# Optimization experiments

Hardware: AMD Instinct MI355X
Metric: run time of the kernel (lower is better)

The kernel has to match this reference:

```python
import jax, jax.numpy as jnp
import numpy as np

NUM_HEADS = 4
GROUPS = 8
EPS = 1e-5


def setup_inputs() -> dict:
    key = jax.random.key(0)
    ks = jax.random.split(key, 8)
    B, C, H, W = 8, 512, 64, 64
    L, E = 77, 768
    std = 0.02
    return {
        "x": jax.random.normal(ks[0], (B, C, H, W), jnp.float32),
        "text_emb": jax.random.normal(ks[1], (B, L, E), jnp.float32),
        "attention_mask": jax.random.randint(ks[2], (B, L), 0, 2, jnp.int32),
        "Wq_w": jax.random.normal(ks[3], (C, C), jnp.float32) * std,
        "Wq_b": jnp.zeros((C,), jnp.float32),
        "Wk_w": jax.random.normal(ks[4], (C, E), jnp.float32) * std,
        "Wk_b": jnp.zeros((C,), jnp.float32),
        "Wv_w": jax.random.normal(ks[5], (C, E), jnp.float32) * std,
        "Wv_b": jnp.zeros((C,), jnp.float32),
        "gn_scale": jnp.ones((C,), jnp.float32),
        "gn_bias": jnp.zeros((C,), jnp.float32),
    }


def reference(x, text_emb, attention_mask, Wq_w, Wq_b, Wk_w, Wk_b, Wv_w, Wv_b, gn_scale, gn_bias):
    B, C, H, W = x.shape
    dh = C // NUM_HEADS
    scale = dh ** -0.5

    # [B, HW, C] queries from image features
    x_flat = x.reshape(B, C, H * W).transpose(0, 2, 1)
    Q = x_flat @ Wq_w.T + Wq_b                 # [B, S, C]
    K = text_emb @ Wk_w.T + Wk_b               # [B, L, C]
    V = text_emb @ Wv_w.T + Wv_b               # [B, L, C]

    def split_heads(t):
        Bt, T, _ = t.shape
        return t.reshape(Bt, T, NUM_HEADS, dh).transpose(0, 2, 1, 3)  # [B, h, T, dh]

    Qh, Kh, Vh = split_heads(Q), split_heads(K), split_heads(V)

    scores = jnp.einsum("bhqd,bhkd->bhqk", Qh, Kh) * scale  # [B, h, S, L]
    mask = (attention_mask == 0)[:, None, None, :]
    scores = jnp.where(mask, -jnp.inf, scores)
    probs = jax.nn.softmax(scores, axis=-1)
    # dropout layers are identity in eval mode
    attn = jnp.einsum("bhqk,bhkd->bhqd", probs, Vh)          # [B, h, S, dh]

    out = attn.transpose(0, 2, 1, 3).reshape(B, H * W, C)    # [B, S, C]
    out = out.transpose(0, 2, 1).reshape(B, C, H, W)

    # GroupNorm(8 groups, affine) over (C/G, H, W) per group
    g = out.reshape(B, GROUPS, -1)
    mean = g.mean(axis=-1, keepdims=True)
    var = g.var(axis=-1, keepdims=True)
    g = (g - mean) * jax.lax.rsqrt(var + EPS)
    out = g.reshape(B, C, H, W) * gn_scale[None, :, None, None] + gn_bias[None, :, None, None]
    return out
```

## Files before the change

kernel.cpp:

```cpp
#include <hip/hip_runtime.h>
#include <hip/hip_bf16.h>
#include <cstdint>


typedef __attribute__((ext_vector_type(8))) short short8;
typedef __attribute__((ext_vector_type(4))) short short4v;
typedef __attribute__((ext_vector_type(4))) float f32x4;

#define DEV __device__ __forceinline__

DEV float bf2f(unsigned short u){ union{uint32_t i; float f;} x; x.i = ((uint32_t)u) << 16; return x.f; }
DEV unsigned short f2bf(float f){ __hip_bfloat16 h = __float2bfloat16(f); return *reinterpret_cast<unsigned short*>(&h); }
DEV short8 ld8(const unsigned short* p){ return *reinterpret_cast<const short8*>(p); }
DEV f32x4 ldf4(const float* p){ return *reinterpret_cast<const f32x4*>(p); }

#if defined(__has_builtin)
#if __has_builtin(__builtin_amdgcn_global_load_lds)
#define HAVE_ASYNC_LDS 1
#endif
#endif

__global__ __launch_bounds__(256) void k_fat(const float* __restrict__ x,
                                             unsigned short* __restrict__ xTt,
                                             const float* __restrict__ text,
                                             const float* __restrict__ Wk,
                                             const float* __restrict__ Wkb,
                                             const float* __restrict__ Wv,
                                             const float* __restrict__ Wvb,
                                             unsigned short* __restrict__ wsK,
                                             unsigned short* __restrict__ wsVt,
                                             const float* __restrict__ Wq,
                                             unsigned short* __restrict__ wsWqT,
                                             int b0, int s_base, int slen, int SB){
  __shared__ unsigned short U[16896];
  const int tid = threadIdx.x;
  const int bx = blockIdx.x, by = blockIdx.y, bz = blockIdx.z;
  const int bg = b0 + bz;

  if (bx >= 3){
    const int cc = by, c0 = cc * 64;
    const int tile = bx - 3;
    const int s0 = s_base + tile * 256;
    {
      const int r = tid >> 2, sub = tid & 3;
      const float* src = &x[((size_t)(bg * 512 + c0 + r)) * 4096 + s0 + sub * 64];
      f32x4 rv[16];
      #pragma unroll
      for (int i = 0; i < 16; ++i) rv[i] = ldf4(src + i * 4);
      unsigned short* drow = &U[r * 264 + sub * 64];
      #pragma unroll
      for (int i = 0; i < 8; ++i){
        short8 v;
        #pragma unroll
        for (int j = 0; j < 4; ++j){ v[j] = (short)f2bf(rv[2*i][j]); v[j + 4] = (short)f2bf(rv[2*i+1][j]); }
        *reinterpret_cast<short8*>(drow + i * 8) = v;
      }
    }
    __syncthreads();
    {
      const int j = tid;
      unsigned short v[64];
      #pragma unroll
      for (int r = 0; r < 64; ++r) v[r] = U[r * 264 + j];
      const int sloc = tile * 256 + j;
      unsigned short* dst = &xTt[(((size_t)bz * 8 + cc) * slen + sloc) * 64];
      #pragma unroll
      for (int g = 0; g < 8; ++g)
        *reinterpret_cast<short8*>(dst + g * 8) = *reinterpret_cast<short8*>(&v[g * 8]);
    }
  } else if (bx < 2){
    unsigned short* At = U;
    unsigned short* Bt = U + 5760;
    const int wave = tid >> 6, lane = tid & 63;
    const int m16 = lane & 15, quad = lane >> 4;
    const int uc = bx * 8 + by;
    const int u0 = uc * 64;
    const bool isK = (u0 < 512);
    const float* W  = isK ? Wk  : Wv;
    const float* Wb = isK ? Wkb : Wvb;
    const int c0 = u0 & 511;
    const int c  = c0 + wave * 16 + m16;

    int srow[9], se4[9]; bool sA[9], sval[9];
    #pragma unroll
    for (int it = 0; it < 9; ++it){
      int slot = tid + it * 256;
      if (slot < 1280){ sA[it] = true;  srow[it] = slot >> 4;          se4[it] = (slot & 15) * 4; sval[it] = (srow[it] < 77); }
      else            { sA[it] = false; srow[it] = (slot - 1280) >> 4; se4[it] = ((slot - 1280) & 15) * 4; sval[it] = true; }
    }
    f32x4 preg[9];
    auto issue = [&](int kc){
      const int e0 = kc * 64;
      #pragma unroll
      for (int it = 0; it < 9; ++it){
        if (sA[it])
          preg[it] = sval[it] ? ldf4(&text[((size_t)(bg * 77 + srow[it])) * 768 + e0 + se4[it]])
                              : (f32x4){0.f, 0.f, 0.f, 0.f};
        else
          preg[it] = ldf4(&W[((size_t)(c0 + srow[it])) * 768 + e0 + se4[it]]);
      }
    };
    auto write_lds = [&](){
      #pragma unroll
      for (int it = 0; it < 9; ++it){
        short4v o;
        #pragma unroll
        for (int j = 0; j < 4; ++j) o[j] = (short)f2bf(preg[it][j]);
        if (sA[it]) *reinterpret_cast<short4v*>(&At[srow[it] * 72 + se4[it]]) = o;
        else        *reinterpret_cast<short4v*>(&Bt[srow[it] * 72 + se4[it]]) = o;
      }
    };

    f32x4 acc[5];
    #pragma unroll
    for (int mt = 0; mt < 5; ++mt) acc[mt] = (f32x4){0.f, 0.f, 0.f, 0.f};
    issue(0);
    for (int kc = 0; kc < 12; ++kc){
      write_lds();
      __syncthreads();
      if (kc < 11) issue(kc + 1);
      #pragma unroll
      for (int kk = 0; kk < 64; kk += 32){
        short8 bf_ = *reinterpret_cast<const short8*>(&Bt[(wave * 16 + m16) * 72 + kk + quad * 8]);
        #pragma unroll
        for (int mt = 0; mt < 5; ++mt){
          short8 af_ = *reinterpret_cast<const short8*>(&At[(mt * 16 + m16) * 72 + kk + quad * 8]);
          acc[mt] = __builtin_amdgcn_mfma_f32_16x16x32_bf16(af_, bf_, acc[mt], 0, 0, 0);
        }
      }
      __syncthreads();
    }
    const float bias = Wb[c];
    if (isK){
      #pragma unroll
      for (int mt = 0; mt < 5; ++mt)
        #pragma unroll
        for (int r = 0; r < 4; ++r){
          int l = mt * 16 + quad * 4 + r;
          if (l < 77) wsK[((size_t)(bz * 77 + l)) * 512 + c] = f2bf(acc[mt][r] + bias);
        }
    } else {
      unsigned short* vr = &wsVt[((size_t)(bz * 512 + c)) * 96];
      #pragma unroll
      for (int mt = 0; mt < 5; ++mt){
        short4v pk;
        #pragma unroll
        for (int r = 0; r < 4; ++r) pk[r] = (short)f2bf(acc[mt][r] + bias);
        *reinterpret_cast<short4v*>(&vr[mt * 16 + quad * 4]) = pk;
      }
      short4v z = {};
      *reinterpret_cast<short4v*>(&vr[80 + quad * 4]) = z;
    }
  } else {
    unsigned short* t = U;
    const int nb = 8 * SB;
    const int p  = by + bz * 8;
    for (int tile = p; tile < 64; tile += nb){
      const int ti = tile >> 3, tj = tile & 7;
      {
        const int r = tid >> 2, sub = tid & 3;
        const float* src = &Wq[((size_t)(tj * 64 + r)) * 512 + ti * 64 + sub * 16];
        f32x4 rv[4];
        #pragma unroll
        for (int i = 0; i < 4; ++i) rv[i] = ldf4(src + i * 4);
        unsigned short* drow = &t[r * 72 + sub * 16];
        #pragma unroll
        for (int i = 0; i < 2; ++i){
          short8 v;
          #pragma unroll
          for (int j = 0; j < 4; ++j){ v[j] = (short)f2bf(rv[2*i][j]); v[j + 4] = (short)f2bf(rv[2*i+1][j]); }
          *reinterpret_cast<short8*>(drow + i * 8) = v;
        }
      }
      __syncthreads();
      #pragma unroll
      for (int it = 0; it < 2; ++it){
        int slot = tid + it * 256;
        int j = slot >> 3, i8 = slot & 7;
        short8 v;
        #pragma unroll
        for (int q = 0; q < 8; ++q)
          v[q] = (short)t[(i8 * 8 + q) * 72 + (j & 63)];
        *reinterpret_cast<short8*>(&wsWqT[((size_t)(ti * 64 + j)) * 512 + tj * 64 + i8 * 8]) = v;
      }
      __syncthreads();
    }
  }
}

__global__ __launch_bounds__(256) void k1b(const unsigned short* __restrict__ wsWqT,
                                           const unsigned short* __restrict__ wsK,
                                           const float* __restrict__ Wqb,
                                           unsigned short* __restrict__ wsKWq,
                                           float* __restrict__ kbias){
  const int tid = threadIdx.x;
  const int wave = tid >> 6, lane = tid & 63;
  const int m16 = lane & 15, quad = lane >> 4;
  const int cq = blockIdx.x, h = blockIdx.y, bz = blockIdx.z;
  const int cbase = cq * 128 + wave * 32;

  f32x4 acc[2][5];
  #pragma unroll
  for (int mt = 0; mt < 2; ++mt)
    #pragma unroll
    for (int nt = 0; nt < 5; ++nt) acc[mt][nt] = (f32x4){0.f, 0.f, 0.f, 0.f};

  #pragma unroll
  for (int ks = 0; ks < 4; ++ks){
    short8 aw[2];
    #pragma unroll
    for (int mt = 0; mt < 2; ++mt)
      aw[mt] = ld8(&wsWqT[(size_t)(cbase + mt * 16 + m16) * 512 + h * 128 + ks * 32 + quad * 8]);
    #pragma unroll
    for (int nt = 0; nt < 5; ++nt){
      int l = nt * 16 + m16;
      short8 bk = {};
      if (l < 77) bk = ld8(&wsK[((size_t)(bz * 77 + l)) * 512 + h * 128 + ks * 32 + quad * 8]);
      #pragma unroll
      for (int mt = 0; mt < 2; ++mt)
        acc[mt][nt] = __builtin_amdgcn_mfma_f32_16x16x32_bf16(aw[mt], bk, acc[mt][nt], 0, 0, 0);
    }
  }
  #pragma unroll
  for (int mt = 0; mt < 2; ++mt)
    #pragma unroll
    for (int nt = 0; nt < 5; ++nt){
      int l = nt * 16 + m16;
      short4v pk;
      #pragma unroll
      for (int r = 0; r < 4; ++r) pk[r] = (short)f2bf(acc[mt][nt][r]);
      *reinterpret_cast<short4v*>(&wsKWq[((size_t)((bz * 4 + h) * 80 + l)) * 512 + cbase + mt * 16 + quad * 4]) = pk;
    }
  if (cq == 0 && tid < 80){
    int l = tid;
    float kb = 0.f;
    if (l < 77){
      #pragma unroll
      for (int d = 0; d < 128; d += 8){
        short8 kv = ld8(&wsK[((size_t)(bz * 77 + l)) * 512 + h * 128 + d]);
        f32x4 wa = ldf4(&Wqb[h * 128 + d]);
        f32x4 wb = ldf4(&Wqb[h * 128 + d + 4]);
        #pragma unroll
        for (int j = 0; j < 4; ++j){
          kb += bf2f((unsigned short)kv[j]) * wa[j];
          kb += bf2f((unsigned short)kv[j + 4]) * wb[j];
        }
      }
    }
    kbias[(bz * 4 + h) * 80 + l] = kb;
  }
}

__global__ __launch_bounds__(256, 4) void k2_attn(const unsigned short* __restrict__ xTt,
                                                  const unsigned short* __restrict__ wsKWq,
                                                  const unsigned short* __restrict__ wsVt,
                                                  const int* __restrict__ amask,
                                                  const float* __restrict__ kbias,
                                                  float* __restrict__ out,
                                                  unsigned short* __restrict__ outTmp,
                                                  float* __restrict__ gnacc,
                                                  int b0, int s_base, int slen, int useTmp){
  __shared__ unsigned short arena[13312];
  __shared__ float maskf[96];
  unsigned short* Pt = arena;

  const int tid = threadIdx.x;
  const int wave = tid >> 6, lane = tid & 63;
  const int m16 = lane & 15, quad = lane >> 4;
  const int bz = blockIdx.x, h = blockIdx.y, st = blockIdx.z;
  const int bg = b0 + bz;
  const int s_glob = s_base + st * 128;
  const int R0 = (wave >> 1) * 64, C0 = (wave & 1) * 64;
  const int sw0 = wave * 32;
  const float scale = 0.08838834764831845f;

  if (tid < 96){
    int l = tid;
    float mbv = -30000.f;
    if (l < 77 && amask[bg * 77 + l] != 0) mbv = kbias[(bz * 4 + h) * 80 + l] * scale;
    maskf[l] = mbv;
  }

  const unsigned short* Abase = wsKWq + (size_t)((bz * 4 + h) * 80) * 512;
  const unsigned short* Bb    = xTt + (size_t)(bz * 8) * slen * 64;
  const int srow0 = st * 128 + sw0;

  f32x4 acc2[5][2];
  #pragma unroll
  for (int mt = 0; mt < 5; ++mt){ acc2[mt][0] = (f32x4){0.f,0.f,0.f,0.f}; acc2[mt][1] = (f32x4){0.f,0.f,0.f,0.f}; }

  auto stageA = [&](int kc, int buf){
    const int sbase = buf * 5120;
    #pragma unroll
    for (int it = 0; it < 3; ++it){
      const int ubase = it * 256 + wave * 64;
      if (ubase < 640){
        const int u = ubase + lane;
        int l = u >> 3, pos = (u & 7) ^ (l & 7);
        const unsigned short* src = Abase + (size_t)l * 512 + kc * 64 + pos * 8;
#ifdef HAVE_ASYNC_LDS
        __builtin_amdgcn_global_load_lds((const __attribute__((address_space(1))) void*)src,
                                         (__attribute__((address_space(3))) void*)&arena[sbase + ubase * 8],
                                         16, 0, 0);
#else
        *reinterpret_cast<short8*>(&arena[sbase + u * 8]) = ld8(src);
#endif
      }
    }
  };

  short8 Breg[2][4];
  auto loadB = [&](int kc, int buf){
    const unsigned short* Bc = Bb + ((size_t)kc * slen + srow0) * 64;
    #pragma unroll
    for (int nt = 0; nt < 2; ++nt)
      #pragma unroll
      for (int kk = 0; kk < 2; ++kk)
        Breg[buf][nt * 2 + kk] = ld8(&Bc[(size_t)(nt * 16 + m16) * 64 + kk * 32 + quad * 8]);
  };

  auto compute = [&](int buf){
    const int ab = buf * 5120;
    #pragma unroll
    for (int kk = 0; kk < 2; ++kk){
      short8 af[5];
      #pragma unroll
      for (int mt = 0; mt < 5; ++mt){
        int l = mt * 16 + m16;
        int p = (kk * 4 + quad) ^ (l & 7);
        af[mt] = *reinterpret_cast<const short8*>(&arena[ab + l * 64 + p * 8]);
      }
      #pragma unroll
      for (int mt = 0; mt < 5; ++mt)
        #pragma unroll
        for (int nt = 0; nt < 2; ++nt)
          acc2[mt][nt] = __builtin_amdgcn_mfma_f32_16x16x32_bf16(af[mt], Breg[buf][nt * 2 + kk], acc2[mt][nt], 0, 0, 0);
    }
  };

  stageA(0, 0);
  loadB(0, 0);
  __syncthreads();
  #pragma unroll
  for (int kc = 0; kc < 8; ++kc){
    if (kc < 7){ stageA(kc + 1, (kc + 1) & 1); loadB(kc + 1, (kc + 1) & 1); }
    compute(kc & 1);
    __syncthreads();
  }

  const unsigned short* Vb = wsVt + (size_t)(bz * 512 + h * 128) * 96;
  short8 av0[4];
  #pragma unroll
  for (int mt = 0; mt < 4; ++mt)
    av0[mt] = ld8(&Vb[(size_t)(R0 + mt * 16 + m16) * 96 + quad * 8]);

  {
    float mb[5][4];
    #pragma unroll
    for (int mt = 0; mt < 5; ++mt)
      #pragma unroll
      for (int r = 0; r < 4; ++r) mb[mt][r] = maskf[mt * 16 + quad * 4 + r];
    #pragma unroll
    for (int nt = 0; nt < 2; ++nt){
      float sv[5][4]; float mx = -3e38f;
      #pragma unroll
      for (int mt = 0; mt < 5; ++mt)
        #pragma unroll
        for (int r = 0; r < 4; ++r){
          float v = acc2[mt][nt][r] * scale + mb[mt][r];
          sv[mt][r] = v; mx = fmaxf(mx, v);
        }
      mx = fmaxf(mx, __shfl_xor(mx, 16)); mx = fmaxf(mx, __shfl_xor(mx, 32));
      float sum = 0.f;
      #pragma unroll
      for (int mt = 0; mt < 5; ++mt)
        #pragma unroll
        for (int r = 0; r < 4; ++r){ float e = __expf(sv[mt][r] - mx); sv[mt][r] = e; sum += e; }
      sum += __shfl_xor(sum, 16); sum += __shfl_xor(sum, 32);
      float inv = 1.0f / sum;
      int sl = sw0 + nt * 16 + m16;
      #pragma unroll
      for (int mt = 0; mt < 5; ++mt){
        short4v pk;
        #pragma unroll
        for (int r = 0; r < 4; ++r) pk[r] = (short)f2bf(sv[mt][r] * inv);
        *reinterpret_cast<short4v*>(&Pt[sl * 104 + mt * 16 + quad * 4]) = pk;
      }
      short4v z = {};
      *reinterpret_cast<short4v*>(&Pt[sl * 104 + 80 + quad * 4]) = z;
    }
  }
  __syncthreads();

  f32x4 acc3[4][4];
  #pragma unroll
  for (int mt = 0; mt < 4; ++mt)
    #pragma unroll
    for (int nt = 0; nt < 4; ++nt) acc3[mt][nt] = (f32x4){0.f, 0.f, 0.f, 0.f};
  #pragma unroll
  for (int ks = 0; ks < 3; ++ks){
    short8 av[4], bp[4];
    #pragma unroll
    for (int mt = 0; mt < 4; ++mt)
      av[mt] = (ks == 0) ? av0[mt]
                         : ld8(&Vb[(size_t)(R0 + mt * 16 + m16) * 96 + ks * 32 + quad * 8]);
    #pragma unroll
    for (int nt = 0; nt < 4; ++nt)
      bp[nt] = *reinterpret_cast<const short8*>(&Pt[(C0 + nt * 16 + m16) * 104 + ks * 32 + quad * 8]);
    #pragma unroll
    for (int mt = 0; mt < 4; ++mt)
      #pragma unroll
      for (int nt = 0; nt < 4; ++nt)
        acc3[mt][nt] = __builtin_amdgcn_mfma_f32_16x16x32_bf16(av[mt], bp[nt], acc3[mt][nt], 0, 0, 0);
  }

  float sum = 0.f, ssq = 0.f;
  #pragma unroll
  for (int mt = 0; mt < 4; ++mt)
    #pragma unroll
    for (int nt = 0; nt < 4; ++nt)
      #pragma unroll
      for (int r = 0; r < 4; ++r){
        float v = acc3[mt][nt][r];
        sum += v; ssq += v * v;
      }
  #pragma unroll
  for (int off = 1; off < 64; off <<= 1){ sum += __shfl_xor(sum, off); ssq += __shfl_xor(ssq, off); }
  if (lane == 0){
    int g = h * 2 + (R0 >> 6);
    atomicAdd(&gnacc[(bg * 8 + g) * 2],     sum);
    atomicAdd(&gnacc[(bg * 8 + g) * 2 + 1], ssq);
  }

  if (useTmp){
    __syncthreads();
    float* T = reinterpret_cast<float*>(arena);
    const int TS = 132;
    #pragma unroll
    for (int p = 0; p < 4; ++p){
      if ((R0 >> 6) == (p >> 1)){
        #pragma unroll
        for (int mt2 = 0; mt2 < 2; ++mt2){
          int mt = (p & 1) * 2 + mt2;
          #pragma unroll
          for (int nt = 0; nt < 4; ++nt)
            #pragma unroll
            for (int r = 0; r < 4; ++r)
              T[(mt2 * 16 + quad * 4 + r) * TS + C0 + nt * 16 + m16] = acc3[mt][nt][r];
        }
      }
      __syncthreads();
      #pragma unroll
      for (int it = 0; it < 4; ++it){
        int row = wave * 8 + it * 2 + (lane >> 5);
        int c = h * 128 + p * 32 + row;
        int sc = (lane & 31) * 4;
        f32x4 v = *reinterpret_cast<const f32x4*>(&T[row * TS + sc]);
        short4v o;
        #pragma unroll
        for (int j = 0; j < 4; ++j) o[j] = (short)f2bf(v[j]);
        *reinterpret_cast<short4v*>(&outTmp[(size_t)(bg * 512 + c) * 4096 + s_glob + sc]) = o;
      }
      __syncthreads();
    }
  } else {
    #pragma unroll
    for (int mt = 0; mt < 4; ++mt)
      #pragma unroll
      for (int nt = 0; nt < 4; ++nt){
        int sidx = s_glob + C0 + nt * 16 + m16;
        #pragma unroll
        for (int r = 0; r < 4; ++r){
          int d = h * 128 + R0 + mt * 16 + quad * 4 + r;
          out[(size_t)(bg * 512 + d) * 4096 + sidx] = acc3[mt][nt][r];
        }
      }
  }
}

__global__ __launch_bounds__(256) void k3_gn_b(const unsigned short* __restrict__ tmp,
                                               float* __restrict__ out,
                                               const float* __restrict__ gnacc,
                                               const float* __restrict__ gns,
                                               const float* __restrict__ gnb){
  const int bx = blockIdx.x;
  const int b = bx >> 9, c = bx & 511;
  const int g = c >> 6;
  const float s  = gnacc[(b * 8 + g) * 2];
  const float ss = gnacc[(b * 8 + g) * 2 + 1];
  const float invN = 1.f / 262144.f;
  const float mean = s * invN;
  const float var  = ss * invN - mean * mean;
  const float rstd = rsqrtf(fmaxf(var, 0.f) + 1e-5f);
  const float a  = rstd * gns[c];
  const float bb = gnb[c] - mean * a;
  const size_t base = (size_t)bx * 4096;
  const unsigned short* src = &tmp[base + threadIdx.x * 16];
  float* dst = &out[base + threadIdx.x * 16];
  short8 v0 = ld8(src), v1 = ld8(src + 8);
  #pragma unroll
  for (int k = 0; k < 2; ++k){
    short8 v = k ? v1 : v0;
    f32x4 o0, o1;
    #pragma unroll
    for (int j = 0; j < 4; ++j){
      o0[j] = bf2f((unsigned short)v[j])     * a + bb;
      o1[j] = bf2f((unsigned short)v[j + 4]) * a + bb;
    }
    *reinterpret_cast<f32x4*>(dst + k * 8)     = o0;
    *reinterpret_cast<f32x4*>(dst + k * 8 + 4) = o1;
  }
}

__global__ __launch_bounds__(256) void k3_gn(float* __restrict__ out,
                                             const float* __restrict__ gnacc,
                                             const float* __restrict__ gns,
                                             const float* __restrict__ gnb){
  const int bx = blockIdx.x;
  const int b = bx >> 9, c = bx & 511;
  const int g = c >> 6;
  const float s  = gnacc[(b * 8 + g) * 2];
  const float ss = gnacc[(b * 8 + g) * 2 + 1];
  const float invN = 1.f / 262144.f;
  const float mean = s * invN;
  const float var  = ss * invN - mean * mean;
  const float rstd = rsqrtf(fmaxf(var, 0.f) + 1e-5f);
  const float a  = rstd * gns[c];
  const float bb = gnb[c] - mean * a;
  const size_t base = (size_t)bx * 4096;
  #pragma unroll
  for (int p = 0; p < 4; ++p){
    size_t off = base + p * 1024 + threadIdx.x * 4;
    f32x4 v = ldf4(&out[off]);
    f32x4 o;
    #pragma unroll
    for (int j = 0; j < 4; ++j) o[j] = v[j] * a + bb;
    *reinterpret_cast<f32x4*>(&out[off]) = o;
  }
}

extern "C" void kernel_launch(void* const* d_in, const int* in_sizes, int n_in,
                              void* d_out, int out_size, void* d_ws, size_t ws_size,
                              hipStream_t stream){
  (void)in_sizes; (void)n_in; (void)out_size;
  const float* x    = (const float*)d_in[0];
  const float* text = (const float*)d_in[1];
  const int*   am   = (const int*)d_in[2];
  const float* Wq   = (const float*)d_in[3];
  const float* Wqb  = (const float*)d_in[4];
  const float* Wk   = (const float*)d_in[5];
  const float* Wkb  = (const float*)d_in[6];
  const float* Wv   = (const float*)d_in[7];
  const float* Wvb  = (const float*)d_in[8];
  const float* gns  = (const float*)d_in[9];
  const float* gnb  = (const float*)d_in[10];
  float* out = (float*)d_out;

  auto need = [](int SB, int SLEN) -> size_t {
    return 512ull + 524288ull + (size_t)SB * 506112ull + (size_t)SB * SLEN * 1024ull;
  };
  int SB = 8, SLEN = 4096;
  if      (ws_size >= need(8, 4096)) { SB = 8; SLEN = 4096; }
  else if (ws_size >= need(4, 4096)) { SB = 4; SLEN = 4096; }
  else if (ws_size >= need(2, 4096)) { SB = 2; SLEN = 4096; }
  else if (ws_size >= need(1, 4096)) { SB = 1; SLEN = 4096; }
  else if (ws_size >= need(1, 1024)) { SB = 1; SLEN = 1024; }
  else                               { SB = 1; SLEN = 256;  }

  const size_t tmpBytes = 8ull * 512 * 4096 * 2;
  const int useTmp = (SB == 8 && SLEN == 4096 && ws_size >= need(8, 4096) + tmpBytes) ? 1 : 0;

  uint8_t* ws = (uint8_t*)d_ws;
  float*          gnacc = (float*)ws;
  unsigned short* wsWqT = (unsigned short*)(ws + 512);
  unsigned short* wsK   = wsWqT + 512 * 512;
  unsigned short* wsVt  = wsK  + (size_t)SB * 77 * 512;
  unsigned short* wsKWq = wsVt + (size_t)SB * 512 * 96;
  float*          kbias = (float*)(wsKWq + (size_t)SB * 4 * 80 * 512);
  unsigned short* xTt   = (unsigned short*)(kbias + (size_t)SB * 4 * 80);
  unsigned short* outTmp = xTt + (size_t)SB * 8 * SLEN * 64;

  hipMemsetAsync(gnacc, 0, 128 * sizeof(float), stream);
  for (int b0 = 0; b0 < 8; b0 += SB){
    for (int s_base = 0; s_base < 4096; s_base += SLEN){
      const int NT = SLEN >> 8;
      k_fat<<<dim3(NT + 3, 8, SB), 256, 0, stream>>>(x, xTt, text, Wk, Wkb, Wv, Wvb,
                                                     wsK, wsVt, Wq, wsWqT, b0, s_base, SLEN, SB);
      if (s_base == 0)
        k1b<<<dim3(4, 4, SB), 256, 0, stream>>>(wsWqT, wsK, Wqb, wsKWq, kbias);
      k2_attn<<<dim3(SB, 4, SLEN / 128), 256, 0, stream>>>(xTt, wsKWq, wsVt, am, kbias,
                                                           out, outTmp, gnacc,
                                                           b0, s_base, SLEN, useTmp);
    }
  }
  if (useTmp)
    k3_gn_b<<<4096, 256, 0, stream>>>(outTmp, out, gnacc, gns, gnb);
  else
    k3_gn<<<4096, 256, 0, stream>>>(out, gnacc, gns, gnb);
}
```

Baseline: 121.1 us.

## Process two heads per attention block to reuse loaded query tiles

Each k2_attn block now handles two heads instead of one. The xTt query tile is loaded into registers once and fed to the score MFMAs of both heads, which halves how often B is read from global memory. The grid's head dimension halves, LDS per block grows to hold two A stages, and launch bounds drop to 2 blocks per CU because the doubled accumulators raise register pressure. The price is lower occupancy and a serial per-head softmax/PV/epilogue section inside each block.

```diff
diff --git a/kernel.cpp b/kernel.cpp
--- a/kernel.cpp
+++ b/kernel.cpp
@@ -251,7 +251,7 @@
   }
 }
 
-__global__ __launch_bounds__(256, 4) void k2_attn(const unsigned short* __restrict__ xTt,
+__global__ __launch_bounds__(256, 2) void k2_attn(const unsigned short* __restrict__ xTt,
                                                   const unsigned short* __restrict__ wsKWq,
                                                   const unsigned short* __restrict__ wsVt,
                                                   const int* __restrict__ amask,
@@ -260,52 +260,61 @@
                                                   unsigned short* __restrict__ outTmp,
                                                   float* __restrict__ gnacc,
                                                   int b0, int s_base, int slen, int useTmp){
-  __shared__ unsigned short arena[13312];
-  __shared__ float maskf[96];
+  __shared__ unsigned short arena[20480];
+  __shared__ float maskf[2][96];
   unsigned short* Pt = arena;
 
   const int tid = threadIdx.x;
   const int wave = tid >> 6, lane = tid & 63;
   const int m16 = lane & 15, quad = lane >> 4;
-  const int bz = blockIdx.x, h = blockIdx.y, st = blockIdx.z;
+  const int bz = blockIdx.x, hp = blockIdx.y, st = blockIdx.z;
   const int bg = b0 + bz;
   const int s_glob = s_base + st * 128;
   const int R0 = (wave >> 1) * 64, C0 = (wave & 1) * 64;
   const int sw0 = wave * 32;
   const float scale = 0.08838834764831845f;
 
-  if (tid < 96){
-    int l = tid;
+  if ((tid & 127) < 96){
+    int hh = tid >> 7, l = tid & 127;
+    int h = hp * 2 + hh;
     float mbv = -30000.f;
     if (l < 77 && amask[bg * 77 + l] != 0) mbv = kbias[(bz * 4 + h) * 80 + l] * scale;
-    maskf[l] = mbv;
-  }
-
-  const unsigned short* Abase = wsKWq + (size_t)((bz * 4 + h) * 80) * 512;
-  const unsigned short* Bb    = xTt + (size_t)(bz * 8) * slen * 64;
+    maskf[hh][l] = mbv;
+  }
+
+  const unsigned short* Ab[2];
+  #pragma unroll
+  for (int hh = 0; hh < 2; ++hh)
+    Ab[hh] = wsKWq + (size_t)((bz * 4 + hp * 2 + hh) * 80) * 512;
+  const unsigned short* Bb = xTt + (size_t)(bz * 8) * slen * 64;
   const int srow0 = st * 128 + sw0;
 
-  f32x4 acc2[5][2];
-  #pragma unroll
-  for (int mt = 0; mt < 5; ++mt){ acc2[mt][0] = (f32x4){0.f,0.f,0.f,0.f}; acc2[mt][1] = (f32x4){0.f,0.f,0.f,0.f}; }
+  f32x4 acc2[2][5][2];
+  #pragma unroll
+  for (int hh = 0; hh < 2; ++hh)
+    #pragma unroll
+    for (int mt = 0; mt < 5; ++mt){
+      acc2[hh][mt][0] = (f32x4){0.f,0.f,0.f,0.f};
+      acc2[hh][mt][1] = (f32x4){0.f,0.f,0.f,0.f};
+    }
 
   auto stageA = [&](int kc, int buf){
-    const int sbase = buf * 5120;
-    #pragma unroll
-    for (int it = 0; it < 3; ++it){
+    const int sbase = buf * 10240;
+    #pragma unroll
+    for (int it = 0; it < 5; ++it){
       const int ubase = it * 256 + wave * 64;
-      if (ubase < 640){
-        const int u = ubase + lane;
-        int l = u >> 3, pos = (u & 7) ^ (l & 7);
-        const unsigned short* src = Abase + (size_t)l * 512 + kc * 64 + pos * 8;
+      const int u = ubase + lane;
+      const int hh = (u >= 640) ? 1 : 0;
+      const int uu = u - hh * 640;
+      int l = uu >> 3, pos = (uu & 7) ^ (l & 7);
+      const unsigned short* src = Ab[hh] + (size_t)l * 512 + kc * 64 + pos * 8;
 #ifdef HAVE_ASYNC_LDS
-        __builtin_amdgcn_global_load_lds((const __attribute__((address_space(1))) void*)src,
-                                         (__attribute__((address_space(3))) void*)&arena[sbase + ubase * 8],
-                                         16, 0, 0);
+      __builtin_amdgcn_global_load_lds((const __attribute__((address_space(1))) void*)src,
+                                       (__attribute__((address_space(3))) void*)&arena[sbase + ubase * 8],
+                                       16, 0, 0);
 #else
-        *reinterpret_cast<short8*>(&arena[sbase + u * 8]) = ld8(src);
+      *reinterpret_cast<short8*>(&arena[sbase + u * 8]) = ld8(src);
 #endif
-      }
     }
   };
 
@@ -320,21 +329,24 @@
   };
 
   auto compute = [&](int buf){
-    const int ab = buf * 5120;
+    const int ab = buf * 10240;
     #pragma unroll
     for (int kk = 0; kk < 2; ++kk){
-      short8 af[5];
-      #pragma unroll
-      for (int mt = 0; mt < 5; ++mt){
-        int l = mt * 16 + m16;
-        int p = (kk * 4 + quad) ^ (l & 7);
-        af[mt] = *reinterpret_cast<const short8*>(&arena[ab + l * 64 + p * 8]);
-      }
-      #pragma unroll
-      for (int mt = 0; mt < 5; ++mt)
-        #pragma unroll
-        for (int nt = 0; nt < 2; ++nt)
-          acc2[mt][nt] = __builtin_amdgcn_mfma_f32_16x16x32_bf16(af[mt], Breg[buf][nt * 2 + kk], acc2[mt][nt], 0, 0, 0);
+      #pragma unroll
+      for (int hh = 0; hh < 2; ++hh){
+        short8 af[5];
+        #pragma unroll
+        for (int mt = 0; mt < 5; ++mt){
+          int l = mt * 16 + m16;
+          int p = (kk * 4 + quad) ^ (l & 7);
+          af[mt] = *reinterpret_cast<const short8*>(&arena[ab + hh * 5120 + l * 64 + p * 8]);
+        }
+        #pragma unroll
+        for (int mt = 0; mt < 5; ++mt)
+          #pragma unroll
+          for (int nt = 0; nt < 2; ++nt)
+            acc2[hh][mt][nt] = __builtin_amdgcn_mfma_f32_16x16x32_bf16(af[mt], Breg[buf][nt * 2 + kk], acc2[hh][mt][nt], 0, 0, 0);
+      }
     }
   };
 
@@ -348,133 +360,138 @@
     __syncthreads();
   }
 
-  const unsigned short* Vb = wsVt + (size_t)(bz * 512 + h * 128) * 96;
-  short8 av0[4];
-  #pragma unroll
-  for (int mt = 0; mt < 4; ++mt)
-    av0[mt] = ld8(&Vb[(size_t)(R0 + mt * 16 + m16) * 96 + quad * 8]);
-
-  {
-    float mb[5][4];
-    #pragma unroll
-    for (int mt = 0; mt < 5; ++mt)
-      #pragma unroll
-      for (int r = 0; r < 4; ++r) mb[mt][r] = maskf[mt * 16 + quad * 4 + r];
-    #pragma unroll
-    for (int nt = 0; nt < 2; ++nt){
-      float sv[5][4]; float mx = -3e38f;
+  #pragma unroll
+  for (int hh = 0; hh < 2; ++hh){
+    const int h = hp * 2 + hh;
+    const unsigned short* Vb = wsVt + (size_t)(bz * 512 + h * 128) * 96;
+    short8 av0[4];
+    #pragma unroll
+    for (int mt = 0; mt < 4; ++mt)
+      av0[mt] = ld8(&Vb[(size_t)(R0 + mt * 16 + m16) * 96 + quad * 8]);
+
+    {
+      float mb[5][4];
       #pragma unroll
       for (int mt = 0; mt < 5; ++mt)
         #pragma unroll
+        for (int r = 0; r < 4; ++r) mb[mt][r] = maskf[hh][mt * 16 + quad * 4 + r];
+      #pragma unroll
+      for (int nt = 0; nt < 2; ++nt){
+        float sv[5][4]; float mx = -3e38f;
+        #pragma unroll
+        for (int mt = 0; mt < 5; ++mt)
+          #pragma unroll
+          for (int r = 0; r < 4; ++r){
+            float v = acc2[hh][mt][nt][r] * scale + mb[mt][r];
+            sv[mt][r] = v; mx = fmaxf(mx, v);
+          }
+        mx = fmaxf(mx, __shfl_xor(mx, 16)); mx = fmaxf(mx, __shfl_xor(mx, 32));
+        float sum = 0.f;
+        #pragma unroll
+        for (int mt = 0; mt < 5; ++mt)
+          #pragma unroll
+          for (int r = 0; r < 4; ++r){ float e = __expf(sv[mt][r] - mx); sv[mt][r] = e; sum += e; }
+        sum += __shfl_xor(sum, 16); sum += __shfl_xor(sum, 32);
+        float inv = 1.0f / sum;
+        int sl = sw0 + nt * 16 + m16;
+        #pragma unroll
+        for (int mt = 0; mt < 5; ++mt){
+          short4v pk;
+          #pragma unroll
+          for (int r = 0; r < 4; ++r) pk[r] = (short)f2bf(sv[mt][r] * inv);
+          *reinterpret_cast<short4v*>(&Pt[sl * 104 + mt * 16 + quad * 4]) = pk;
+        }
+        short4v z = {};
+        *reinterpret_cast<short4v*>(&Pt[sl * 104 + 80 + quad * 4]) = z;
+      }
+    }
+    __syncthreads();
+
+    f32x4 acc3[4][4];
+    #pragma unroll
+    for (int mt = 0; mt < 4; ++mt)
+      #pragma unroll
+      for (int nt = 0; nt < 4; ++nt) acc3[mt][nt] = (f32x4){0.f, 0.f, 0.f, 0.f};
+    #pragma unroll
+    for (int ks = 0; ks < 3; ++ks){
+      short8 av[4], bp[4];
+      #pragma unroll
+      for (int mt = 0; mt < 4; ++mt)
+        av[mt] = (ks == 0) ? av0[mt]
+                           : ld8(&Vb[(size_t)(R0 + mt * 16 + m16) * 96 + ks * 32 + quad * 8]);
+      #pragma unroll
+      for (int nt = 0; nt < 4; ++nt)
+        bp[nt] = *reinterpret_cast<const short8*>(&Pt[(C0 + nt * 16 + m16) * 104 + ks * 32 + quad * 8]);
+      #pragma unroll
+      for (int mt = 0; mt < 4; ++mt)
+        #pragma unroll
+        for (int nt = 0; nt < 4; ++nt)
+          acc3[mt][nt] = __builtin_amdgcn_mfma_f32_16x16x32_bf16(av[mt], bp[nt], acc3[mt][nt], 0, 0, 0);
+    }
+
+    float sum = 0.f, ssq = 0.f;
+    #pragma unroll
+    for (int mt = 0; mt < 4; ++mt)
+      #pragma unroll
+      for (int nt = 0; nt < 4; ++nt)
+        #pragma unroll
         for (int r = 0; r < 4; ++r){
-          float v = acc2[mt][nt][r] * scale + mb[mt][r];
-          sv[mt][r] = v; mx = fmaxf(mx, v);
-        }
-      mx = fmaxf(mx, __shfl_xor(mx, 16)); mx = fmaxf(mx, __shfl_xor(mx, 32));
-      float sum = 0.f;
-      #pragma unroll
-      for (int mt = 0; mt < 5; ++mt)
-        #pragma unroll
-        for (int r = 0; r < 4; ++r){ float e = __expf(sv[mt][r] - mx); sv[mt][r] = e; sum += e; }
-      sum += __shfl_xor(sum, 16); sum += __shfl_xor(sum, 32);
-      float inv = 1.0f / sum;
-      int sl = sw0 + nt * 16 + m16;
-      #pragma unroll
-      for (int mt = 0; mt < 5; ++mt){
-        short4v pk;
-        #pragma unroll
-        for (int r = 0; r < 4; ++r) pk[r] = (short)f2bf(sv[mt][r] * inv);
-        *reinterpret_cast<short4v*>(&Pt[sl * 104 + mt * 16 + quad * 4]) = pk;
-      }
-      short4v z = {};
-      *reinterpret_cast<short4v*>(&Pt[sl * 104 + 80 + quad * 4]) = z;
-    }
-  }
-  __syncthreads();
-
-  f32x4 acc3[4][4];
-  #pragma unroll
-  for (int mt = 0; mt < 4; ++mt)
-    #pragma unroll
-    for (int nt = 0; nt < 4; ++nt) acc3[mt][nt] = (f32x4){0.f, 0.f, 0.f, 0.f};
-  #pragma unroll
-  for (int ks = 0; ks < 3; ++ks){
-    short8 av[4], bp[4];
-    #pragma unroll
-    for (int mt = 0; mt < 4; ++mt)
-      av[mt] = (ks == 0) ? av0[mt]
-                         : ld8(&Vb[(size_t)(R0 + mt * 16 + m16) * 96 + ks * 32 + quad * 8]);
-    #pragma unroll
-    for (int nt = 0; nt < 4; ++nt)
-      bp[nt] = *reinterpret_cast<const short8*>(&Pt[(C0 + nt * 16 + m16) * 104 + ks * 32 + quad * 8]);
-    #pragma unroll
-    for (int mt = 0; mt < 4; ++mt)
-      #pragma unroll
-      for (int nt = 0; nt < 4; ++nt)
-        acc3[mt][nt] = __builtin_amdgcn_mfma_f32_16x16x32_bf16(av[mt], bp[nt], acc3[mt][nt], 0, 0, 0);
-  }
-
-  float sum = 0.f, ssq = 0.f;
-  #pragma unroll
-  for (int mt = 0; mt < 4; ++mt)
-    #pragma unroll
-    for (int nt = 0; nt < 4; ++nt)
-      #pragma unroll
-      for (int r = 0; r < 4; ++r){
-        float v = acc3[mt][nt][r];
-        sum += v; ssq += v * v;
-      }
-  #pragma unroll
-  for (int off = 1; off < 64; off <<= 1){ sum += __shfl_xor(sum, off); ssq += __shfl_xor(ssq, off); }
-  if (lane == 0){
-    int g = h * 2 + (R0 >> 6);
-    atomicAdd(&gnacc[(bg * 8 + g) * 2],     sum);
-    atomicAdd(&gnacc[(bg * 8 + g) * 2 + 1], ssq);
-  }
-
-  if (useTmp){
-    __syncthreads();
-    float* T = reinterpret_cast<float*>(arena);
-    const int TS = 132;
-    #pragma unroll
-    for (int p = 0; p < 4; ++p){
-      if ((R0 >> 6) == (p >> 1)){
-        #pragma unroll
-        for (int mt2 = 0; mt2 < 2; ++mt2){
-          int mt = (p & 1) * 2 + mt2;
-          #pragma unroll
-          for (int nt = 0; nt < 4; ++nt)
+          float v = acc3[mt][nt][r];
+          sum += v; ssq += v * v;
+        }
+    #pragma unroll
+    for (int off = 1; off < 64; off <<= 1){ sum += __shfl_xor(sum, off); ssq += __shfl_xor(ssq, off); }
+    if (lane == 0){
+      int g = h * 2 + (R0 >> 6);
+      atomicAdd(&gnacc[(bg * 8 + g) * 2],     sum);
+      atomicAdd(&gnacc[(bg * 8 + g) * 2 + 1], ssq);
+    }
+
+    if (useTmp){
+      __syncthreads();
+      float* T = reinterpret_cast<float*>(arena);
+      const int TS = 132;
+      #pragma unroll
+      for (int p = 0; p < 4; ++p){
+        if ((R0 >> 6) == (p >> 1)){
+          #pragma unroll
+          for (int mt2 = 0; mt2 < 2; ++mt2){
+            int mt = (p & 1) * 2 + mt2;
             #pragma unroll
-            for (int r = 0; r < 4; ++r)
-              T[(mt2 * 16 + quad * 4 + r) * TS + C0 + nt * 16 + m16] = acc3[mt][nt][r];
-        }
-      }
+            for (int nt = 0; nt < 4; ++nt)
+              #pragma unroll
+              for (int r = 0; r < 4; ++r)
+                T[(mt2 * 16 + quad * 4 + r) * TS + C0 + nt * 16 + m16] = acc3[mt][nt][r];
+          }
+        }
+        __syncthreads();
+        #pragma unroll
+        for (int it = 0; it < 4; ++it){
+          int row = wave * 8 + it * 2 + (lane >> 5);
+          int c = h * 128 + p * 32 + row;
+          int sc = (lane & 31) * 4;
+          f32x4 v = *reinterpret_cast<const f32x4*>(&T[row * TS + sc]);
+          short4v o;
+          #pragma unroll
+          for (int j = 0; j < 4; ++j) o[j] = (short)f2bf(v[j]);
+          *reinterpret_cast<short4v*>(&outTmp[(size_t)(bg * 512 + c) * 4096 + s_glob + sc]) = o;
+        }
+        __syncthreads();
+      }
+    } else {
+      #pragma unroll
+      for (int mt = 0; mt < 4; ++mt)
+        #pragma unroll
+        for (int nt = 0; nt < 4; ++nt){
+          int sidx = s_glob + C0 + nt * 16 + m16;
+          #pragma unroll
+          for (int r = 0; r < 4; ++r){
+            int d = h * 128 + R0 + mt * 16 + quad * 4 + r;
+            out[(size_t)(bg * 512 + d) * 4096 + sidx] = acc3[mt][nt][r];
+          }
+        }
       __syncthreads();
-      #pragma unroll
-      for (int it = 0; it < 4; ++it){
-        int row = wave * 8 + it * 2 + (lane >> 5);
-        int c = h * 128 + p * 32 + row;
-        int sc = (lane & 31) * 4;
-        f32x4 v = *reinterpret_cast<const f32x4*>(&T[row * TS + sc]);
-        short4v o;
-        #pragma unroll
-        for (int j = 0; j < 4; ++j) o[j] = (short)f2bf(v[j]);
-        *reinterpret_cast<short4v*>(&outTmp[(size_t)(bg * 512 + c) * 4096 + s_glob + sc]) = o;
-      }
-      __syncthreads();
-    }
-  } else {
-    #pragma unroll
-    for (int mt = 0; mt < 4; ++mt)
-      #pragma unroll
-      for (int nt = 0; nt < 4; ++nt){
-        int sidx = s_glob + C0 + nt * 16 + m16;
-        #pragma unroll
-        for (int r = 0; r < 4; ++r){
-          int d = h * 128 + R0 + mt * 16 + quad * 4 + r;
-          out[(size_t)(bg * 512 + d) * 4096 + sidx] = acc3[mt][nt][r];
-        }
-      }
+    }
   }
 }
 
@@ -588,7 +605,7 @@
                                                      wsK, wsVt, Wq, wsWqT, b0, s_base, SLEN, SB);
       if (s_base == 0)
         k1b<<<dim3(4, 4, SB), 256, 0, stream>>>(wsWqT, wsK, Wqb, wsKWq, kbias);
-      k2_attn<<<dim3(SB, 4, SLEN / 128), 256, 0, stream>>>(xTt, wsKWq, wsVt, am, kbias,
+      k2_attn<<<dim3(SB, 2, SLEN / 128), 256, 0, stream>>>(xTt, wsKWq, wsVt, am, kbias,
                                                            out, outTmp, gnacc,
                                                            b0, s_base, SLEN, useTmp);
     }
```

New measurement: 117.8 us (median of 2 runs). 2.6% less time.

## Stage full K·Wq tile in LDS once and drop per-chunk barriers in score GEMM

Applied to the files above, without the earlier changes.

The attention kernel now loads the whole 80x512 bf16 K·Wq slab for the head into LDS with one async batch, where before it double-buffered 64-wide chunks with a barrier after each. The B operand (image features) is prefetched four chunks ahead in registers, and the mask bias is computed directly into registers instead of going through shared memory. This removes seven block barriers and the per-chunk staging latency in the QK phase. In exchange, LDS per block grows to about 80KB and the launch bound drops to 2 blocks per CU, which lowers occupancy and raises register pressure.

```diff
diff --git a/kernel.cpp b/kernel.cpp
--- a/kernel.cpp
+++ b/kernel.cpp
@@ -251,7 +251,7 @@
   }
 }
 
-__global__ __launch_bounds__(256, 4) void k2_attn(const unsigned short* __restrict__ xTt,
+__global__ __launch_bounds__(256, 2) void k2_attn(const unsigned short* __restrict__ xTt,
                                                   const unsigned short* __restrict__ wsKWq,
                                                   const unsigned short* __restrict__ wsVt,
                                                   const int* __restrict__ amask,
@@ -260,8 +260,7 @@
                                                   unsigned short* __restrict__ outTmp,
                                                   float* __restrict__ gnacc,
                                                   int b0, int s_base, int slen, int useTmp){
-  __shared__ unsigned short arena[13312];
-  __shared__ float maskf[96];
+  __shared__ unsigned short arena[40960];
   unsigned short* Pt = arena;
 
   const int tid = threadIdx.x;
@@ -274,79 +273,78 @@
   const int sw0 = wave * 32;
   const float scale = 0.08838834764831845f;
 
-  if (tid < 96){
-    int l = tid;
-    float mbv = -30000.f;
-    if (l < 77 && amask[bg * 77 + l] != 0) mbv = kbias[(bz * 4 + h) * 80 + l] * scale;
-    maskf[l] = mbv;
-  }
-
   const unsigned short* Abase = wsKWq + (size_t)((bz * 4 + h) * 80) * 512;
   const unsigned short* Bb    = xTt + (size_t)(bz * 8) * slen * 64;
   const int srow0 = st * 128 + sw0;
 
+  #pragma unroll
+  for (int i = 0; i < 20; ++i){
+    const int ubase = i * 256 + wave * 64;
+    const int u = ubase + lane;
+    const int l = u >> 6, pos = u & 63;
+    const unsigned short* src = Abase + (size_t)l * 512 + (pos ^ (l & 7)) * 8;
+#ifdef HAVE_ASYNC_LDS
+    __builtin_amdgcn_global_load_lds((const __attribute__((address_space(1))) void*)src,
+                                     (__attribute__((address_space(3))) void*)&arena[ubase * 8],
+                                     16, 0, 0);
+#else
+    *reinterpret_cast<short8*>(&arena[u * 8]) = ld8(src);
+#endif
+  }
+
+  short8 Breg[4][4];
+  auto loadB = [&](int kc, int slot){
+    const unsigned short* Bc = Bb + ((size_t)kc * slen + srow0) * 64;
+    #pragma unroll
+    for (int nt = 0; nt < 2; ++nt)
+      #pragma unroll
+      for (int kk = 0; kk < 2; ++kk)
+        Breg[slot][nt * 2 + kk] = ld8(&Bc[(size_t)(nt * 16 + m16) * 64 + kk * 32 + quad * 8]);
+  };
+  #pragma unroll
+  for (int c4 = 0; c4 < 4; ++c4) loadB(c4, c4);
+
+  float mb[5][4];
+  #pragma unroll
+  for (int mt = 0; mt < 5; ++mt)
+    #pragma unroll
+    for (int r = 0; r < 4; ++r){
+      int l = mt * 16 + quad * 4 + r;
+      float v = -30000.f;
+      if (l < 77 && amask[bg * 77 + l] != 0) v = kbias[(bz * 4 + h) * 80 + l] * scale;
+      mb[mt][r] = v;
+    }
+
   f32x4 acc2[5][2];
   #pragma unroll
   for (int mt = 0; mt < 5; ++mt){ acc2[mt][0] = (f32x4){0.f,0.f,0.f,0.f}; acc2[mt][1] = (f32x4){0.f,0.f,0.f,0.f}; }
 
-  auto stageA = [&](int kc, int buf){
-    const int sbase = buf * 5120;
-    #pragma unroll
-    for (int it = 0; it < 3; ++it){
-      const int ubase = it * 256 + wave * 64;
-      if (ubase < 640){
-        const int u = ubase + lane;
-        int l = u >> 3, pos = (u & 7) ^ (l & 7);
-        const unsigned short* src = Abase + (size_t)l * 512 + kc * 64 + pos * 8;
-#ifdef HAVE_ASYNC_LDS
-        __builtin_amdgcn_global_load_lds((const __attribute__((address_space(1))) void*)src,
-                                         (__attribute__((address_space(3))) void*)&arena[sbase + ubase * 8],
-                                         16, 0, 0);
-#else
-        *reinterpret_cast<short8*>(&arena[sbase + u * 8]) = ld8(src);
-#endif
-      }
-    }
-  };
-
-  short8 Breg[2][4];
-  auto loadB = [&](int kc, int buf){
-    const unsigned short* Bc = Bb + ((size_t)kc * slen + srow0) * 64;
-    #pragma unroll
-    for (int nt = 0; nt < 2; ++nt)
-      #pragma unroll
-      for (int kk = 0; kk < 2; ++kk)
-        Breg[buf][nt * 2 + kk] = ld8(&Bc[(size_t)(nt * 16 + m16) * 64 + kk * 32 + quad * 8]);
-  };
-
-  auto compute = [&](int buf){
-    const int ab = buf * 5120;
+  auto compute = [&](int kc, int slot){
     #pragma unroll
     for (int kk = 0; kk < 2; ++kk){
       short8 af[5];
       #pragma unroll
       for (int mt = 0; mt < 5; ++mt){
         int l = mt * 16 + m16;
-        int p = (kk * 4 + quad) ^ (l & 7);
-        af[mt] = *reinterpret_cast<const short8*>(&arena[ab + l * 64 + p * 8]);
+        int gs = (kc * 8 + kk * 4 + quad) ^ (l & 7);
+        af[mt] = *reinterpret_cast<const short8*>(&arena[l * 512 + gs * 8]);
       }
       #pragma unroll
       for (int mt = 0; mt < 5; ++mt)
         #pragma unroll
         for (int nt = 0; nt < 2; ++nt)
-          acc2[mt][nt] = __builtin_amdgcn_mfma_f32_16x16x32_bf16(af[mt], Breg[buf][nt * 2 + kk], acc2[mt][nt], 0, 0, 0);
+          acc2[mt][nt] = __builtin_amdgcn_mfma_f32_16x16x32_bf16(af[mt], Breg[slot][nt * 2 + kk], acc2[mt][nt], 0, 0, 0);
     }
   };
 
-  stageA(0, 0);
-  loadB(0, 0);
   __syncthreads();
-  #pragma unroll
-  for (int kc = 0; kc < 8; ++kc){
-    if (kc < 7){ stageA(kc + 1, (kc + 1) & 1); loadB(kc + 1, (kc + 1) & 1); }
-    compute(kc & 1);
-    __syncthreads();
-  }
+
+  #pragma unroll
+  for (int kc = 0; kc < 4; ++kc) compute(kc, kc);
+  #pragma unroll
+  for (int kc = 4; kc < 8; ++kc) loadB(kc, kc - 4);
+  #pragma unroll
+  for (int kc = 4; kc < 8; ++kc) compute(kc, kc - 4);
 
   const unsigned short* Vb = wsVt + (size_t)(bz * 512 + h * 128) * 96;
   short8 av0[4];
@@ -354,41 +352,36 @@
   for (int mt = 0; mt < 4; ++mt)
     av0[mt] = ld8(&Vb[(size_t)(R0 + mt * 16 + m16) * 96 + quad * 8]);
 
-  {
-    float mb[5][4];
+  __syncthreads();
+
+  #pragma unroll
+  for (int nt = 0; nt < 2; ++nt){
+    float sv[5][4]; float mx = -3e38f;
     #pragma unroll
     for (int mt = 0; mt < 5; ++mt)
       #pragma unroll
-      for (int r = 0; r < 4; ++r) mb[mt][r] = maskf[mt * 16 + quad * 4 + r];
-    #pragma unroll
-    for (int nt = 0; nt < 2; ++nt){
-      float sv[5][4]; float mx = -3e38f;
-      #pragma unroll
-      for (int mt = 0; mt < 5; ++mt)
-        #pragma unroll
-        for (int r = 0; r < 4; ++r){
-          float v = acc2[mt][nt][r] * scale + mb[mt][r];
-          sv[mt][r] = v; mx = fmaxf(mx, v);
-        }
-      mx = fmaxf(mx, __shfl_xor(mx, 16)); mx = fmaxf(mx, __shfl_xor(mx, 32));
-      float sum = 0.f;
-      #pragma unroll
-      for (int mt = 0; mt < 5; ++mt)
-        #pragma unroll
-        for (int r = 0; r < 4; ++r){ float e = __expf(sv[mt][r] - mx); sv[mt][r] = e; sum += e; }
-      sum += __shfl_xor(sum, 16); sum += __shfl_xor(sum, 32);
-      float inv = 1.0f / sum;
-      int sl = sw0 + nt * 16 + m16;
-      #pragma unroll
-      for (int mt = 0; mt < 5; ++mt){
-        short4v pk;
-        #pragma unroll
-        for (int r = 0; r < 4; ++r) pk[r] = (short)f2bf(sv[mt][r] * inv);
-        *reinterpret_cast<short4v*>(&Pt[sl * 104 + mt * 16 + quad * 4]) = pk;
-      }
-      short4v z = {};
-      *reinterpret_cast<short4v*>(&Pt[sl * 104 + 80 + quad * 4]) = z;
-    }
+      for (int r = 0; r < 4; ++r){
+        float v = acc2[mt][nt][r] * scale + mb[mt][r];
+        sv[mt][r] = v; mx = fmaxf(mx, v);
+      }
+    mx = fmaxf(mx, __shfl_xor(mx, 16)); mx = fmaxf(mx, __shfl_xor(mx, 32));
+    float sum = 0.f;
+    #pragma unroll
+    for (int mt = 0; mt < 5; ++mt)
+      #pragma unroll
+      for (int r = 0; r < 4; ++r){ float e = __expf(sv[mt][r] - mx); sv[mt][r] = e; sum += e; }
+    sum += __shfl_xor(sum, 16); sum += __shfl_xor(sum, 32);
+    float inv = 1.0f / sum;
+    int sl = sw0 + nt * 16 + m16;
+    #pragma unroll
+    for (int mt = 0; mt < 5; ++mt){
+      short4v pk;
+      #pragma unroll
+      for (int r = 0; r < 4; ++r) pk[r] = (short)f2bf(sv[mt][r] * inv);
+      *reinterpret_cast<short4v*>(&Pt[sl * 104 + mt * 16 + quad * 4]) = pk;
+    }
+    short4v z = {};
+    *reinterpret_cast<short4v*>(&Pt[sl * 104 + 80 + quad * 4]) = z;
   }
   __syncthreads();
 
```

Result: slower. 123.6 us (+2.1%).
